# Kernel optimization log

Hardware: AMD Instinct MI355X
Metric: run time of the kernel (lower is better)

Reference implementation:

```python
import jax, jax.numpy as jnp
import numpy as np
from jax import lax

BN_EPS = 1e-5
PAD = ((2, 3), (1, 2))  # 'same' padding for kernel (6,4): H pad 5 -> (2,3), W pad 3 -> (1,2)
DN = ('NCHW', 'OIHW', 'NCHW')


def _conv_block(x, w, b, g, bt, m, v, pool):
    # pool(bn(relu(conv(pad(x))))) as in the torch module (eval-mode BN)
    x = lax.conv_general_dilated(x, w, (1, 1), PAD, dimension_numbers=DN)
    x = jax.nn.relu(x + b[None, :, None, None])
    scale = g / jnp.sqrt(v + BN_EPS)
    x = (x - m[None, :, None, None]) * scale[None, :, None, None] + bt[None, :, None, None]
    win = (1, 1) + pool
    return lax.reduce_window(x, -jnp.inf, lax.max, win, win, 'VALID')


def _fc_bn(x, w, b, g, bt, m, v):
    x = jax.nn.relu(x @ w.T + b)
    return (x - m) * (g / jnp.sqrt(v + BN_EPS)) + bt


def _apply_cnn(x, p):
    x = x[:, None, :, :]  # [N,1,72,64]
    x = _conv_block(x, p['conv1_w'], p['conv1_b'], p['bnc1_g'], p['bnc1_b'], p['bnc1_m'], p['bnc1_v'], (2, 2))
    x = _conv_block(x, p['conv2_w'], p['conv2_b'], p['bnc2_g'], p['bnc2_b'], p['bnc2_m'], p['bnc2_v'], (2, 2))
    x = _conv_block(x, p['conv3_w'], p['conv3_b'], p['bnc3_g'], p['bnc3_b'], p['bnc3_m'], p['bnc3_v'], (3, 4))
    x = x.reshape(x.shape[0], 6 * 4 * 64)  # NCHW contiguous flatten matches torch .view
    x = _fc_bn(x, p['fc1_w'], p['fc1_b'], p['bnf1_g'], p['bnf1_b'], p['bnf1_m'], p['bnf1_v'])
    x = _fc_bn(x, p['fc2_w'], p['fc2_b'], p['bnf2_g'], p['bnf2_b'], p['bnf2_m'], p['bnf2_v'])
    x = _fc_bn(x, p['fc3_w'], p['fc3_b'], p['bnf3_g'], p['bnf3_b'], p['bnf3_m'], p['bnf3_v'])
    # F.normalize(x, p=2, dim=1) with eps=1e-12
    nrm = jnp.linalg.norm(x, axis=1, keepdims=True)
    return x / jnp.maximum(nrm, 1e-12)


def _ssm(embeds):
    # pairwise L2 distances via Gram trick (replaces the O(n^2) python loop)
    sq = jnp.sum(embeds * embeds, axis=1)  # [n]
    d2 = sq[:, None] + sq[None, :] - 2.0 * (embeds @ embeds.T)
    dist = jnp.sqrt(jnp.maximum(d2, 1e-12))
    dist = jnp.where(d2 > 0, dist, 0.0)  # exact zeros on diagonal, nan-safe grad
    return dist / jnp.max(dist)


def setup_inputs() -> dict:
    key = jax.random.key(0)
    ks = iter(jax.random.split(key, 64))
    d = {'x': jax.random.normal(next(ks), (512, 72, 64), jnp.float32)}

    def nrm(shape, s=0.05):
        return jax.random.normal(next(ks), shape, jnp.float32) * s

    def add_bn(name, c):
        d[name + '_g'] = 1.0 + nrm((c,))
        d[name + '_b'] = nrm((c,))
        d[name + '_m'] = nrm((c,), 0.1)
        d[name + '_v'] = 0.5 + jax.random.uniform(next(ks), (c,), jnp.float32)

    d['conv1_w'] = nrm((16, 1, 6, 4), 0.2);  d['conv1_b'] = nrm((16,));  add_bn('bnc1', 16)
    d['conv2_w'] = nrm((32, 16, 6, 4), 0.1); d['conv2_b'] = nrm((32,));  add_bn('bnc2', 32)
    d['conv3_w'] = nrm((64, 32, 6, 4), 0.05); d['conv3_b'] = nrm((64,)); add_bn('bnc3', 64)
    d['fc1_w'] = nrm((512, 1536), 0.03); d['fc1_b'] = nrm((512,)); add_bn('bnf1', 512)
    d['fc2_w'] = nrm((256, 512), 0.05);  d['fc2_b'] = nrm((256,)); add_bn('bnf2', 256)
    d['fc3_w'] = nrm((128, 256), 0.07);  d['fc3_b'] = nrm((128,)); add_bn('bnf3', 128)
    return d


def reference(x,
              conv1_w, conv1_b, bnc1_g, bnc1_b, bnc1_m, bnc1_v,
              conv2_w, conv2_b, bnc2_g, bnc2_b, bnc2_m, bnc2_v,
              conv3_w, conv3_b, bnc3_g, bnc3_b, bnc3_m, bnc3_v,
              fc1_w, fc1_b, bnf1_g, bnf1_b, bnf1_m, bnf1_v,
              fc2_w, fc2_b, bnf2_g, bnf2_b, bnf2_m, bnf2_v,
              fc3_w, fc3_b, bnf3_g, bnf3_b, bnf3_m, bnf3_v):
    p = dict(conv1_w=conv1_w, conv1_b=conv1_b, bnc1_g=bnc1_g, bnc1_b=bnc1_b, bnc1_m=bnc1_m, bnc1_v=bnc1_v,
             conv2_w=conv2_w, conv2_b=conv2_b, bnc2_g=bnc2_g, bnc2_b=bnc2_b, bnc2_m=bnc2_m, bnc2_v=bnc2_v,
             conv3_w=conv3_w, conv3_b=conv3_b, bnc3_g=bnc3_g, bnc3_b=bnc3_b, bnc3_m=bnc3_m, bnc3_v=bnc3_v,
             fc1_w=fc1_w, fc1_b=fc1_b, bnf1_g=bnf1_g, bnf1_b=bnf1_b, bnf1_m=bnf1_m, bnf1_v=bnf1_v,
             fc2_w=fc2_w, fc2_b=fc2_b, bnf2_g=bnf2_g, bnf2_b=bnf2_b, bnf2_m=bnf2_m, bnf2_v=bnf2_v,
             fc3_w=fc3_w, fc3_b=fc3_b, bnf3_g=bnf3_g, bnf3_b=bnf3_b, bnf3_m=bnf3_m, bnf3_v=bnf3_v)
    embeds = _apply_cnn(x, p)  # [n, 128], L2-normalized
    return _ssm(embeds)        # [n, n]
```

## Files before the change

### kernel.cpp

```cpp
#include <hip/hip_runtime.h>
#include <math.h>


#define BN_EPS 1e-5f

typedef __attribute__((ext_vector_type(8))) short short8;
typedef __attribute__((ext_vector_type(4))) float f32x4;

__device__ __forceinline__ unsigned short f2bf(float f) {
    unsigned u = __float_as_uint(f);
    u += 0x7fffu + ((u >> 16) & 1u);
    return (unsigned short)(u >> 16);
}

__global__ __launch_bounds__(256) void repack_k(
    const float* __restrict__ w1, const float* __restrict__ w2,
    const float* __restrict__ w3,
    const float* __restrict__ fw1, const float* __restrict__ fw2,
    const float* __restrict__ fw3,
    unsigned short* __restrict__ wT1b,
    unsigned short* __restrict__ wT2b, unsigned short* __restrict__ wT3b,
    unsigned short* __restrict__ fw1b, unsigned short* __restrict__ fw2b,
    unsigned short* __restrict__ fw3b, unsigned* __restrict__ mxslot)
{
    int t = blockIdx.x * 256 + threadIdx.x;
    if (t == 0) *mxslot = 0u;
    if (t < 512) {
        int k = t & 31, oc = t >> 5;
        wT1b[t] = (k < 24) ? f2bf(w1[oc * 24 + k]) : (unsigned short)0;
    }
    if (t < 12288) {
        int k = t & 31, oc = (t >> 5) & 31, kk = t >> 10;
        int ky = kk >> 1, kxp = kk & 1;
        int hi = k >> 4, ic = k & 15;
        int kx = 2 * kxp + hi;
        wT2b[t] = f2bf(w2[((oc * 16 + ic) * 6 + ky) * 4 + kx]);
    }
    if (t < 49152) {
        int ic = t & 31, oc = (t >> 5) & 63, kk = t >> 11;
        int ky = kk >> 2, kx = kk & 3;
        wT3b[t] = f2bf(w3[((oc * 32 + ic) * 6 + ky) * 4 + kx]);
    }
    if (t < 786432) fw1b[t] = f2bf(fw1[t]);
    if (t < 131072) fw2b[t] = f2bf(fw2[t]);
    if (t < 32768)  fw3b[t] = f2bf(fw3[t]);
}

__global__ __launch_bounds__(512) void conv_all(
    const float* __restrict__ x, const unsigned short* __restrict__ wT1,
    const unsigned short* __restrict__ wT2, const unsigned short* __restrict__ wT3,
    const float* __restrict__ c1b, const float* __restrict__ g1,
    const float* __restrict__ b1, const float* __restrict__ m1,
    const float* __restrict__ v1,
    const float* __restrict__ c2b, const float* __restrict__ g2,
    const float* __restrict__ b2, const float* __restrict__ m2,
    const float* __restrict__ v2,
    const float* __restrict__ c3b, const float* __restrict__ g3,
    const float* __restrict__ b3, const float* __restrict__ m3,
    const float* __restrict__ v3,
    unsigned short* __restrict__ out3)
{
    __shared__ __align__(16) unsigned short s_out1[41 * 36 * 16];
    __shared__ __align__(16) unsigned short s_un[24 * 20 * 32];
    const int tid = threadIdx.x, nl = blockIdx.x;
    const int lane = tid & 63, wave = tid >> 6;
    const int n = lane & 15, q = lane >> 4;
    unsigned short* pa = s_un;
    unsigned short* pb = s_un + 5372;

    {
        unsigned* z32 = (unsigned*)s_un;
        for (int i = tid; i < 5372; i += 512) z32[i] = 0u;
        uint4 z4; z4.x = z4.y = z4.z = z4.w = 0u;
        for (int pc = tid; pc < 324; pc += 512) {
            int row, colc;
            if (pc < 180) { row = pc / 36; colc = pc % 36; if (row >= 2) row += 36; }
            else { int pz = pc - 180; row = 2 + (pz >> 2); colc = (pz & 3) ? 32 + (pz & 3) : 0; }
            uint4* d = (uint4*)(s_out1 + ((size_t)row * 36 + colc) * 16);
            d[0] = z4; d[1] = z4;
        }
    }
    __syncthreads();
    {
        const float4* src = (const float4*)(x + (size_t)nl * 4608);
        for (int i = tid; i < 1152; i += 512) {
            float4 val = src[i];
            int f = i * 4, row = (f >> 6) + 2, c = (f & 63) + 1;
            unsigned short h0 = f2bf(val.x), h1 = f2bf(val.y);
            unsigned short h2 = f2bf(val.z), h3 = f2bf(val.w);
            unsigned short* ap = pa + row * 68 + c;
            ap[0] = h0; ap[1] = h1; ap[2] = h2; ap[3] = h3;
            unsigned* bp = (unsigned*)(pb + row * 68 + c + 1);
            bp[0] = (unsigned)h0 | ((unsigned)h1 << 16);
            bp[1] = (unsigned)h2 | ((unsigned)h3 << 16);
        }
    }
    const float sc1 = g1[n] * rsqrtf(v1[n] + BN_EPS);
    const float bb1 = c1b[n];
    const float mm1 = b1[n] - m1[n] * sc1;
    const short8 bfr1 = *(const short8*)(wT1 + n * 32 + q * 8);
    __syncthreads();

    for (int i = 0; i < 36; ++i) {
        int t = wave * 36 + i;
        int pooled = 4 * t + (n >> 2);
        int ph = pooled >> 5, pw = pooled & 31;
        int py = (n >> 1) & 1, px = n & 1;
        int oh = 2 * ph + py, ow = 2 * pw + px;
        int r0 = (oh + 2 * q) * 68;
        const unsigned* base = px ? (const unsigned*)(pb + r0 + ow + 1)
                                  : (const unsigned*)(pa + r0 + ow);
        uint4 uu;
        uu.x = base[0];  uu.y = base[1];
        uu.z = base[34]; uu.w = base[35];
        short8 afr = *reinterpret_cast<short8*>(&uu);
        f32x4 acc = (f32x4){0.f, 0.f, 0.f, 0.f};
        acc = __builtin_amdgcn_mfma_f32_16x16x32_bf16(afr, bfr1, acc, 0, 0, 0);
        int po = 4 * t + q, oph = po >> 5, opw = po & 31;
        float mx = fmaxf(fmaxf(acc[0], acc[1]), fmaxf(acc[2], acc[3]));
        float val = fmaxf(mx + bb1, 0.f) * sc1 + mm1;
        s_out1[((oph + 2) * 36 + (opw + 1)) * 16 + n] = f2bf(val);
    }
    __syncthreads();
    {
        uint4 z4; z4.x = z4.y = z4.z = z4.w = 0u;
        for (int pc = tid; pc < 192; pc += 512) {
            int row, colc;
            if (pc < 120) { row = pc / 20; colc = pc % 20; if (row >= 2) row += 18; }
            else { int pz = pc - 120; row = 2 + (pz >> 2); colc = (pz & 3) ? 16 + (pz & 3) : 0; }
            uint4* d = (uint4*)(s_un + ((size_t)row * 20 + colc) * 32);
            d[0] = z4; d[1] = z4; d[2] = z4; d[3] = z4;
        }
    }
    float bnb2[2], bns2[2], bnm2[2];
#pragma unroll
    for (int nt = 0; nt < 2; ++nt) {
        int oc = nt * 16 + n;
        float sc = g2[oc] * rsqrtf(v2[oc] + BN_EPS);
        bnb2[nt] = c2b[oc]; bns2[nt] = sc; bnm2[nt] = b2[oc] - m2[oc] * sc;
    }
    __syncthreads();

    for (int pp = wave; pp < 36; pp += 8) {
        int ph = pp >> 1, half = pp & 1;
        f32x4 acc[2][2];
#pragma unroll
        for (int ab = 0; ab < 2; ++ab)
#pragma unroll
            for (int nt = 0; nt < 2; ++nt) acc[ab][nt] = (f32x4){0.f, 0.f, 0.f, 0.f};
#pragma unroll
        for (int ky = 0; ky < 6; ++ky)
#pragma unroll
            for (int kxp = 0; kxp < 2; ++kxp) {
                int kk = ky * 2 + kxp;
                short8 w0 = *(const short8*)(wT2 + ((size_t)(kk * 32 + n) * 32) + q * 8);
                short8 w1 = *(const short8*)(wT2 + ((size_t)(kk * 32 + 16 + n) * 32) + q * 8);
                int col = half * 16 + n + 2 * kxp;
#pragma unroll
                for (int ab = 0; ab < 2; ++ab) {
                    int row = 2 * ph + ab + ky;
                    short8 afr = *(const short8*)(s_out1 + ((size_t)(row * 36 + col) * 16) + q * 8);
                    acc[ab][0] = __builtin_amdgcn_mfma_f32_16x16x32_bf16(afr, w0, acc[ab][0], 0, 0, 0);
                    acc[ab][1] = __builtin_amdgcn_mfma_f32_16x16x32_bf16(afr, w1, acc[ab][1], 0, 0, 0);
                }
            }
        int pw0 = half * 8 + q * 2;
#pragma unroll
        for (int nt = 0; nt < 2; ++nt) {
            int oc = nt * 16 + n;
            float p0 = fmaxf(fmaxf(acc[0][nt][0], acc[0][nt][1]),
                             fmaxf(acc[1][nt][0], acc[1][nt][1]));
            float p1 = fmaxf(fmaxf(acc[0][nt][2], acc[0][nt][3]),
                             fmaxf(acc[1][nt][2], acc[1][nt][3]));
            p0 = fmaxf(p0 + bnb2[nt], 0.f) * bns2[nt] + bnm2[nt];
            p1 = fmaxf(p1 + bnb2[nt], 0.f) * bns2[nt] + bnm2[nt];
            s_un[((size_t)(ph + 2) * 20 + (pw0 + 1)) * 32 + oc] = f2bf(p0);
            s_un[((size_t)(ph + 2) * 20 + (pw0 + 2)) * 32 + oc] = f2bf(p1);
        }
    }
    __syncthreads();

    for (int ch = wave; ch < 12; ch += 8) {
        int pr = ch >> 1, nth = ch & 1;
        f32x4 acc[3][2];
#pragma unroll
        for (int r = 0; r < 3; ++r)
#pragma unroll
            for (int t2 = 0; t2 < 2; ++t2) acc[r][t2] = (f32x4){0.f, 0.f, 0.f, 0.f};
#pragma unroll
        for (int ky = 0; ky < 6; ++ky)
#pragma unroll
            for (int kx = 0; kx < 4; ++kx) {
                int kk = ky * 4 + kx;
                short8 w0 = *(const short8*)(wT3 + ((size_t)(kk * 64 + nth * 32 + n) * 32) + q * 8);
                short8 w1 = *(const short8*)(wT3 + ((size_t)(kk * 64 + nth * 32 + 16 + n) * 32) + q * 8);
#pragma unroll
                for (int r = 0; r < 3; ++r) {
                    int row = 3 * pr + r + ky;
                    int col = n + kx;
                    short8 afr = *(const short8*)(s_un + ((size_t)(row * 20 + col) * 32) + q * 8);
                    acc[r][0] = __builtin_amdgcn_mfma_f32_16x16x32_bf16(afr, w0, acc[r][0], 0, 0, 0);
                    acc[r][1] = __builtin_amdgcn_mfma_f32_16x16x32_bf16(afr, w1, acc[r][1], 0, 0, 0);
                }
            }
        size_t ob = (size_t)nl * 1536;
#pragma unroll
        for (int t2 = 0; t2 < 2; ++t2) {
            int oc = nth * 32 + t2 * 16 + n;
            float sc = g3[oc] * rsqrtf(v3[oc] + BN_EPS);
            float mx = -3.4e38f;
#pragma unroll
            for (int r = 0; r < 3; ++r)
#pragma unroll
                for (int e = 0; e < 4; ++e) mx = fmaxf(mx, acc[r][t2][e]);
            float val = fmaxf(mx + c3b[oc], 0.f) * sc + (b3[oc] - m3[oc] * sc);
            out3[ob + (size_t)oc * 24 + pr * 4 + q] = f2bf(val);
        }
    }
}

__global__ __launch_bounds__(256) void fc_m(
    const unsigned short* __restrict__ A, const unsigned short* __restrict__ W,
    const float* __restrict__ bias, const float* __restrict__ g,
    const float* __restrict__ bt, const float* __restrict__ m,
    const float* __restrict__ v, unsigned short* __restrict__ out_b,
    float* __restrict__ out_f, int K, int N, int mode)
{
    const int tid = threadIdx.x;
    const int lane = tid & 63, wave = tid >> 6;
    const int n = lane & 15, q = lane >> 4;
    const int wr = wave >> 1, wc = wave & 1;
    const int r0 = blockIdx.y * 32 + wr * 16;
    const int c0 = blockIdx.x * 32 + wc * 16;
    const int col = c0 + n;

    float sc = g[col] * rsqrtf(v[col] + BN_EPS);
    float bb = bias[col];
    float mm = bt[col] - m[col] * sc;

    const unsigned short* Ap = A + (size_t)(r0 + n) * K + q * 8;
    const unsigned short* Bp = W + (size_t)col * K + q * 8;

    f32x4 acc = (f32x4){0.f, 0.f, 0.f, 0.f};
    for (int kk = 0; kk < K; kk += 64) {
        short8 a0 = *(const short8*)(Ap + kk);
        short8 b0 = *(const short8*)(Bp + kk);
        short8 a1 = *(const short8*)(Ap + kk + 32);
        short8 b1 = *(const short8*)(Bp + kk + 32);
        acc = __builtin_amdgcn_mfma_f32_16x16x32_bf16(a0, b0, acc, 0, 0, 0);
        acc = __builtin_amdgcn_mfma_f32_16x16x32_bf16(a1, b1, acc, 0, 0, 0);
    }
#pragma unroll
    for (int e = 0; e < 4; ++e) {
        int row = r0 + q * 4 + e;
        float val = fmaxf(acc[e] + bb, 0.f) * sc + mm;
        if (mode == 0) out_b[(size_t)row * N + col] = f2bf(val);
        else           out_f[(size_t)row * N + col] = val;
    }
}

__global__ __launch_bounds__(128) void norm_k(const float* __restrict__ f3,
                                              float* __restrict__ E,
                                              float* __restrict__ sq)
{
    __shared__ float red[2];
    const int row = blockIdx.x, tid = threadIdx.x;
    float vv = f3[row * 128 + tid];
    float s = vv * vv;
#pragma unroll
    for (int off = 32; off >= 1; off >>= 1) s += __shfl_down(s, off, 64);
    if ((tid & 63) == 0) red[tid >> 6] = s;
    __syncthreads();
    float total = red[0] + red[1];
    float nn = fmaxf(sqrtf(total), 1e-12f);
    E[row * 128 + tid] = vv / nn;
    if (tid == 0) sq[row] = total / (nn * nn);
}

__global__ __launch_bounds__(256) void dist_k(const float* __restrict__ E,
                                              const float* __restrict__ sq,
                                              float* __restrict__ D,
                                              unsigned* __restrict__ mxslot)
{
    __shared__ __align__(16) float Ei[16 * 132];
    __shared__ __align__(16) float Ej[16 * 132];
    __shared__ float red[256];
    const int tid = threadIdx.x;
    const int bi = blockIdx.y * 16, bj = blockIdx.x * 16;
    {
        int lr = tid >> 4, lc = (tid & 15) * 8;
        float4 a0 = *(const float4*)(E + (bi + lr) * 128 + lc);
        float4 a1 = *(const float4*)(E + (bi + lr) * 128 + lc + 4);
        *(float4*)(Ei + lr * 132 + lc) = a0;
        *(float4*)(Ei + lr * 132 + lc + 4) = a1;
        float4 b0 = *(const float4*)(E + (bj + lr) * 128 + lc);
        float4 b1 = *(const float4*)(E + (bj + lr) * 128 + lc + 4);
        *(float4*)(Ej + lr * 132 + lc) = b0;
        *(float4*)(Ej + lr * 132 + lc + 4) = b1;
    }
    __syncthreads();
    const int tx = tid & 15, ty = tid >> 4;
    float dot = 0.f;
#pragma unroll 4
    for (int k = 0; k < 128; k += 4) {
        float4 a = *(const float4*)(Ei + ty * 132 + k);
        float4 b = *(const float4*)(Ej + tx * 132 + k);
        dot = fmaf(a.x, b.x, dot); dot = fmaf(a.y, b.y, dot);
        dot = fmaf(a.z, b.z, dot); dot = fmaf(a.w, b.w, dot);
    }
    int i = bi + ty, j = bj + tx;
    float d2 = sq[i] + sq[j] - 2.f * dot;
    float dist = sqrtf(fmaxf(d2, 1e-12f));
    dist = (d2 > 0.f) ? dist : 0.f;
    if (i == j) dist = 0.f;
    D[i * 512 + j] = dist;
    red[tid] = dist;
    __syncthreads();
    for (int s2 = 128; s2 > 0; s2 >>= 1) {
        if (tid < s2) red[tid] = fmaxf(red[tid], red[tid + s2]);
        __syncthreads();
    }
    if (tid == 0) atomicMax(mxslot, __float_as_uint(red[0]));
}

__global__ __launch_bounds__(256) void scale_k(float* __restrict__ D,
                                               const unsigned* __restrict__ mxslot)
{
    int idx = blockIdx.x * 256 + threadIdx.x;
    float M = __uint_as_float(*mxslot);
    D[idx] = D[idx] / M;
}

extern "C" void kernel_launch(void* const* d_in, const int* in_sizes, int n_in,
                              void* d_out, int out_size, void* d_ws, size_t ws_size,
                              hipStream_t stream)
{
    (void)in_sizes; (void)n_in; (void)out_size; (void)ws_size;
    const float* x    = (const float*)d_in[0];
    const float* c1w  = (const float*)d_in[1];
    const float* c1b  = (const float*)d_in[2];
    const float* g1   = (const float*)d_in[3];
    const float* b1   = (const float*)d_in[4];
    const float* m1   = (const float*)d_in[5];
    const float* v1   = (const float*)d_in[6];
    const float* c2w  = (const float*)d_in[7];
    const float* c2b  = (const float*)d_in[8];
    const float* g2   = (const float*)d_in[9];
    const float* b2   = (const float*)d_in[10];
    const float* m2   = (const float*)d_in[11];
    const float* v2   = (const float*)d_in[12];
    const float* c3w  = (const float*)d_in[13];
    const float* c3b  = (const float*)d_in[14];
    const float* g3   = (const float*)d_in[15];
    const float* b3   = (const float*)d_in[16];
    const float* m3   = (const float*)d_in[17];
    const float* v3   = (const float*)d_in[18];
    const float* fw1  = (const float*)d_in[19];
    const float* fb1  = (const float*)d_in[20];
    const float* gf1  = (const float*)d_in[21];
    const float* bf1  = (const float*)d_in[22];
    const float* mf1  = (const float*)d_in[23];
    const float* vf1  = (const float*)d_in[24];
    const float* fw2  = (const float*)d_in[25];
    const float* fb2  = (const float*)d_in[26];
    const float* gf2  = (const float*)d_in[27];
    const float* bf2  = (const float*)d_in[28];
    const float* mf2  = (const float*)d_in[29];
    const float* vf2  = (const float*)d_in[30];
    const float* fw3  = (const float*)d_in[31];
    const float* fb3  = (const float*)d_in[32];
    const float* gf3  = (const float*)d_in[33];
    const float* bf3  = (const float*)d_in[34];
    const float* mf3  = (const float*)d_in[35];
    const float* vf3  = (const float*)d_in[36];

    float* ws = (float*)d_ws;
    float* E    = ws + 0;
    float* sq   = ws + 65536;
    float* f3v  = ws + 66048;
    unsigned* mx = (unsigned*)(ws + 131584);
    unsigned short* wT1b = (unsigned short*)(ws + 131600);
    unsigned short* wT2b = (unsigned short*)(ws + 131856);
    unsigned short* wT3b = (unsigned short*)(ws + 138000);
    unsigned short* fw1b = (unsigned short*)(ws + 162576);
    unsigned short* fw2b = (unsigned short*)(ws + 555792);
    unsigned short* fw3b = (unsigned short*)(ws + 621328);
    unsigned short* out3b= (unsigned short*)(ws + 637712);
    unsigned short* a1b  = (unsigned short*)(ws + 1030928);
    unsigned short* a2b  = (unsigned short*)(ws + 1162000);

    float* out = (float*)d_out;

    repack_k<<<3072, 256, 0, stream>>>(c1w, c2w, c3w, fw1, fw2, fw3,
                                       wT1b, wT2b, wT3b, fw1b, fw2b, fw3b, mx);
    conv_all<<<512, 512, 0, stream>>>(x, wT1b, wT2b, wT3b,
                                      c1b, g1, b1, m1, v1,
                                      c2b, g2, b2, m2, v2,
                                      c3b, g3, b3, m3, v3, out3b);
    fc_m<<<dim3(16, 16), 256, 0, stream>>>(out3b, fw1b, fb1, gf1, bf1, mf1, vf1,
                                           a1b, nullptr, 1536, 512, 0);
    fc_m<<<dim3(8, 16), 256, 0, stream>>>(a1b, fw2b, fb2, gf2, bf2, mf2, vf2,
                                          a2b, nullptr, 512, 256, 0);
    fc_m<<<dim3(4, 16), 256, 0, stream>>>(a2b, fw3b, fb3, gf3, bf3, mf3, vf3,
                                          nullptr, f3v, 256, 128, 1);
    norm_k<<<512, 128, 0, stream>>>(f3v, E, sq);
    dist_k<<<dim3(32, 32), 256, 0, stream>>>(E, sq, out, mx);
    scale_k<<<1024, 256, 0, stream>>>(out, mx);
}
```

Measured before the change: 219.6 us.

## Convert FC weights in-kernel, fuse fc3 with normalize, swizzle conv3 LDS, resize conv block

Stops pre-converting the large FC weight matrices to bf16 in the repack kernel. The FC kernels now read fp32 weights and pack them to bf16 in registers, which removes a big write and re-read pass over the weights. The final FC layer is fused with L2 normalisation into one kernel, which drops the separate norm launch and its intermediate buffer. The conv kernel moves from 512 to 384 threads, with work redistributed per wave and an XOR-swizzled LDS layout for conv2's output / conv3's input to avoid bank conflicts. The cost is extra global fp32 weight traffic and conversion work repeated in every FC block, since each weight tile is read by many row blocks.

New measurement: 229.2 us. 1.04x slower.

```diff
diff --git a/kernel.cpp b/kernel.cpp
--- a/kernel.cpp
+++ b/kernel.cpp
@@ -1,4 +1,5 @@
 #include <hip/hip_runtime.h>
+#include <hip/hip_bf16.h>
 #include <math.h>
 
 
@@ -13,15 +14,21 @@
     return (unsigned short)(u >> 16);
 }
 
+__device__ __forceinline__ unsigned pkbf(float a, float b) {
+    __hip_bfloat162 h = __float22bfloat162_rn(make_float2(a, b));
+    return *reinterpret_cast<unsigned*>(&h);
+}
+
+__device__ __forceinline__ int sw2(int c, int h) {
+    return c * 32 + ((h ^ (c & 3) ^ ((c >> 2) & 3)) << 3);
+}
+
 __global__ __launch_bounds__(256) void repack_k(
     const float* __restrict__ w1, const float* __restrict__ w2,
     const float* __restrict__ w3,
-    const float* __restrict__ fw1, const float* __restrict__ fw2,
-    const float* __restrict__ fw3,
     unsigned short* __restrict__ wT1b,
     unsigned short* __restrict__ wT2b, unsigned short* __restrict__ wT3b,
-    unsigned short* __restrict__ fw1b, unsigned short* __restrict__ fw2b,
-    unsigned short* __restrict__ fw3b, unsigned* __restrict__ mxslot)
+    unsigned* __restrict__ mxslot)
 {
     int t = blockIdx.x * 256 + threadIdx.x;
     if (t == 0) *mxslot = 0u;
@@ -41,12 +48,9 @@
         int ky = kk >> 2, kx = kk & 3;
         wT3b[t] = f2bf(w3[((oc * 32 + ic) * 6 + ky) * 4 + kx]);
     }
-    if (t < 786432) fw1b[t] = f2bf(fw1[t]);
-    if (t < 131072) fw2b[t] = f2bf(fw2[t]);
-    if (t < 32768)  fw3b[t] = f2bf(fw3[t]);
-}
-
-__global__ __launch_bounds__(512) void conv_all(
+}
+
+__global__ __launch_bounds__(384) void conv_all(
     const float* __restrict__ x, const unsigned short* __restrict__ wT1,
     const unsigned short* __restrict__ wT2, const unsigned short* __restrict__ wT3,
     const float* __restrict__ c1b, const float* __restrict__ g1,
@@ -70,9 +74,9 @@
 
     {
         unsigned* z32 = (unsigned*)s_un;
-        for (int i = tid; i < 5372; i += 512) z32[i] = 0u;
+        for (int i = tid; i < 5372; i += 384) z32[i] = 0u;
         uint4 z4; z4.x = z4.y = z4.z = z4.w = 0u;
-        for (int pc = tid; pc < 324; pc += 512) {
+        for (int pc = tid; pc < 324; pc += 384) {
             int row, colc;
             if (pc < 180) { row = pc / 36; colc = pc % 36; if (row >= 2) row += 36; }
             else { int pz = pc - 180; row = 2 + (pz >> 2); colc = (pz & 3) ? 32 + (pz & 3) : 0; }
@@ -83,7 +87,7 @@
     __syncthreads();
     {
         const float4* src = (const float4*)(x + (size_t)nl * 4608);
-        for (int i = tid; i < 1152; i += 512) {
+        for (int i = tid; i < 1152; i += 384) {
             float4 val = src[i];
             int f = i * 4, row = (f >> 6) + 2, c = (f & 63) + 1;
             unsigned short h0 = f2bf(val.x), h1 = f2bf(val.y);
@@ -101,8 +105,8 @@
     const short8 bfr1 = *(const short8*)(wT1 + n * 32 + q * 8);
     __syncthreads();
 
-    for (int i = 0; i < 36; ++i) {
-        int t = wave * 36 + i;
+    for (int i = 0; i < 48; ++i) {
+        int t = wave * 48 + i;
         int pooled = 4 * t + (n >> 2);
         int ph = pooled >> 5, pw = pooled & 31;
         int py = (n >> 1) & 1, px = n & 1;
@@ -124,7 +128,7 @@
     __syncthreads();
     {
         uint4 z4; z4.x = z4.y = z4.z = z4.w = 0u;
-        for (int pc = tid; pc < 192; pc += 512) {
+        for (int pc = tid; pc < 192; pc += 384) {
             int row, colc;
             if (pc < 120) { row = pc / 20; colc = pc % 20; if (row >= 2) row += 18; }
             else { int pz = pc - 120; row = 2 + (pz >> 2); colc = (pz & 3) ? 16 + (pz & 3) : 0; }
@@ -141,7 +145,7 @@
     }
     __syncthreads();
 
-    for (int pp = wave; pp < 36; pp += 8) {
+    for (int pp = wave; pp < 36; pp += 6) {
         int ph = pp >> 1, half = pp & 1;
         f32x4 acc[2][2];
 #pragma unroll
@@ -174,57 +178,50 @@
                              fmaxf(acc[1][nt][2], acc[1][nt][3]));
             p0 = fmaxf(p0 + bnb2[nt], 0.f) * bns2[nt] + bnm2[nt];
             p1 = fmaxf(p1 + bnb2[nt], 0.f) * bns2[nt] + bnm2[nt];
-            s_un[((size_t)(ph + 2) * 20 + (pw0 + 1)) * 32 + oc] = f2bf(p0);
-            s_un[((size_t)(ph + 2) * 20 + (pw0 + 2)) * 32 + oc] = f2bf(p1);
+            int c1 = (ph + 2) * 20 + (pw0 + 1);
+            s_un[sw2(c1, oc >> 3) + (oc & 7)] = f2bf(p0);
+            s_un[sw2(c1 + 1, oc >> 3) + (oc & 7)] = f2bf(p1);
         }
     }
     __syncthreads();
 
-    for (int ch = wave; ch < 12; ch += 8) {
-        int pr = ch >> 1, nth = ch & 1;
-        f32x4 acc[3][2];
-#pragma unroll
-        for (int r = 0; r < 3; ++r)
-#pragma unroll
-            for (int t2 = 0; t2 < 2; ++t2) acc[r][t2] = (f32x4){0.f, 0.f, 0.f, 0.f};
+    for (int u = wave; u < 24; u += 6) {
+        int pr = u >> 2, nt4 = u & 3;
+        f32x4 acc[3];
+#pragma unroll
+        for (int r = 0; r < 3; ++r) acc[r] = (f32x4){0.f, 0.f, 0.f, 0.f};
 #pragma unroll
         for (int ky = 0; ky < 6; ++ky)
 #pragma unroll
             for (int kx = 0; kx < 4; ++kx) {
                 int kk = ky * 4 + kx;
-                short8 w0 = *(const short8*)(wT3 + ((size_t)(kk * 64 + nth * 32 + n) * 32) + q * 8);
-                short8 w1 = *(const short8*)(wT3 + ((size_t)(kk * 64 + nth * 32 + 16 + n) * 32) + q * 8);
+                short8 w0 = *(const short8*)(wT3 + ((size_t)(kk * 64 + nt4 * 16 + n) * 32) + q * 8);
 #pragma unroll
                 for (int r = 0; r < 3; ++r) {
                     int row = 3 * pr + r + ky;
-                    int col = n + kx;
-                    short8 afr = *(const short8*)(s_un + ((size_t)(row * 20 + col) * 32) + q * 8);
-                    acc[r][0] = __builtin_amdgcn_mfma_f32_16x16x32_bf16(afr, w0, acc[r][0], 0, 0, 0);
-                    acc[r][1] = __builtin_amdgcn_mfma_f32_16x16x32_bf16(afr, w1, acc[r][1], 0, 0, 0);
+                    int c = row * 20 + n + kx;
+                    short8 afr = *(const short8*)(s_un + sw2(c, q));
+                    acc[r] = __builtin_amdgcn_mfma_f32_16x16x32_bf16(afr, w0, acc[r], 0, 0, 0);
                 }
             }
-        size_t ob = (size_t)nl * 1536;
-#pragma unroll
-        for (int t2 = 0; t2 < 2; ++t2) {
-            int oc = nth * 32 + t2 * 16 + n;
-            float sc = g3[oc] * rsqrtf(v3[oc] + BN_EPS);
-            float mx = -3.4e38f;
-#pragma unroll
-            for (int r = 0; r < 3; ++r)
-#pragma unroll
-                for (int e = 0; e < 4; ++e) mx = fmaxf(mx, acc[r][t2][e]);
-            float val = fmaxf(mx + c3b[oc], 0.f) * sc + (b3[oc] - m3[oc] * sc);
-            out3[ob + (size_t)oc * 24 + pr * 4 + q] = f2bf(val);
-        }
+        int oc = nt4 * 16 + n;
+        float sc = g3[oc] * rsqrtf(v3[oc] + BN_EPS);
+        float mx = -3.4e38f;
+#pragma unroll
+        for (int r = 0; r < 3; ++r)
+#pragma unroll
+            for (int e = 0; e < 4; ++e) mx = fmaxf(mx, acc[r][e]);
+        float val = fmaxf(mx + c3b[oc], 0.f) * sc + (b3[oc] - m3[oc] * sc);
+        out3[(size_t)nl * 1536 + (size_t)oc * 24 + pr * 4 + q] = f2bf(val);
     }
 }
 
 __global__ __launch_bounds__(256) void fc_m(
-    const unsigned short* __restrict__ A, const unsigned short* __restrict__ W,
+    const unsigned short* __restrict__ A, const float* __restrict__ Wf,
     const float* __restrict__ bias, const float* __restrict__ g,
     const float* __restrict__ bt, const float* __restrict__ m,
     const float* __restrict__ v, unsigned short* __restrict__ out_b,
-    float* __restrict__ out_f, int K, int N, int mode)
+    int K, int N)
 {
     const int tid = threadIdx.x;
     const int lane = tid & 63, wave = tid >> 6;
@@ -239,14 +236,23 @@
     float mm = bt[col] - m[col] * sc;
 
     const unsigned short* Ap = A + (size_t)(r0 + n) * K + q * 8;
-    const unsigned short* Bp = W + (size_t)col * K + q * 8;
+    const float* Bp = Wf + (size_t)col * K + q * 8;
 
     f32x4 acc = (f32x4){0.f, 0.f, 0.f, 0.f};
     for (int kk = 0; kk < K; kk += 64) {
         short8 a0 = *(const short8*)(Ap + kk);
-        short8 b0 = *(const short8*)(Bp + kk);
         short8 a1 = *(const short8*)(Ap + kk + 32);
-        short8 b1 = *(const short8*)(Bp + kk + 32);
+        float4 f0 = *(const float4*)(Bp + kk);
+        float4 f1 = *(const float4*)(Bp + kk + 4);
+        float4 f2 = *(const float4*)(Bp + kk + 32);
+        float4 f3 = *(const float4*)(Bp + kk + 36);
+        uint4 u0, u1;
+        u0.x = pkbf(f0.x, f0.y); u0.y = pkbf(f0.z, f0.w);
+        u0.z = pkbf(f1.x, f1.y); u0.w = pkbf(f1.z, f1.w);
+        u1.x = pkbf(f2.x, f2.y); u1.y = pkbf(f2.z, f2.w);
+        u1.z = pkbf(f3.x, f3.y); u1.w = pkbf(f3.z, f3.w);
+        short8 b0 = *reinterpret_cast<short8*>(&u0);
+        short8 b1 = *reinterpret_cast<short8*>(&u1);
         acc = __builtin_amdgcn_mfma_f32_16x16x32_bf16(a0, b0, acc, 0, 0, 0);
         acc = __builtin_amdgcn_mfma_f32_16x16x32_bf16(a1, b1, acc, 0, 0, 0);
     }
@@ -254,27 +260,73 @@
     for (int e = 0; e < 4; ++e) {
         int row = r0 + q * 4 + e;
         float val = fmaxf(acc[e] + bb, 0.f) * sc + mm;
-        if (mode == 0) out_b[(size_t)row * N + col] = f2bf(val);
-        else           out_f[(size_t)row * N + col] = val;
-    }
-}
-
-__global__ __launch_bounds__(128) void norm_k(const float* __restrict__ f3,
-                                              float* __restrict__ E,
-                                              float* __restrict__ sq)
-{
-    __shared__ float red[2];
-    const int row = blockIdx.x, tid = threadIdx.x;
-    float vv = f3[row * 128 + tid];
-    float s = vv * vv;
-#pragma unroll
-    for (int off = 32; off >= 1; off >>= 1) s += __shfl_down(s, off, 64);
-    if ((tid & 63) == 0) red[tid >> 6] = s;
-    __syncthreads();
-    float total = red[0] + red[1];
-    float nn = fmaxf(sqrtf(total), 1e-12f);
-    E[row * 128 + tid] = vv / nn;
-    if (tid == 0) sq[row] = total / (nn * nn);
+        out_b[(size_t)row * N + col] = f2bf(val);
+    }
+}
+
+__global__ __launch_bounds__(512) void fc3norm_k(
+    const unsigned short* __restrict__ A, const float* __restrict__ Wf,
+    const float* __restrict__ bias, const float* __restrict__ g,
+    const float* __restrict__ bt, const float* __restrict__ m,
+    const float* __restrict__ v,
+    float* __restrict__ E, float* __restrict__ sq)
+{
+    __shared__ __align__(16) float z3[16 * 128];
+    const int tid = threadIdx.x;
+    const int lane = tid & 63, wave = tid >> 6;
+    const int n = lane & 15, q = lane >> 4;
+    const int r0 = blockIdx.x * 16;
+    const int col = wave * 16 + n;
+
+    float sc = g[col] * rsqrtf(v[col] + BN_EPS);
+    float bb = bias[col];
+    float mm = bt[col] - m[col] * sc;
+
+    const unsigned short* Ap = A + (size_t)(r0 + n) * 256 + q * 8;
+    const float* Bp = Wf + (size_t)col * 256 + q * 8;
+
+    f32x4 acc = (f32x4){0.f, 0.f, 0.f, 0.f};
+    for (int kk = 0; kk < 256; kk += 64) {
+        short8 a0 = *(const short8*)(Ap + kk);
+        short8 a1 = *(const short8*)(Ap + kk + 32);
+        float4 f0 = *(const float4*)(Bp + kk);
+        float4 f1 = *(const float4*)(Bp + kk + 4);
+        float4 f2 = *(const float4*)(Bp + kk + 32);
+        float4 f3 = *(const float4*)(Bp + kk + 36);
+        uint4 u0, u1;
+        u0.x = pkbf(f0.x, f0.y); u0.y = pkbf(f0.z, f0.w);
+        u0.z = pkbf(f1.x, f1.y); u0.w = pkbf(f1.z, f1.w);
+        u1.x = pkbf(f2.x, f2.y); u1.y = pkbf(f2.z, f2.w);
+        u1.z = pkbf(f3.x, f3.y); u1.w = pkbf(f3.z, f3.w);
+        short8 b0 = *reinterpret_cast<short8*>(&u0);
+        short8 b1 = *reinterpret_cast<short8*>(&u1);
+        acc = __builtin_amdgcn_mfma_f32_16x16x32_bf16(a0, b0, acc, 0, 0, 0);
+        acc = __builtin_amdgcn_mfma_f32_16x16x32_bf16(a1, b1, acc, 0, 0, 0);
+    }
+#pragma unroll
+    for (int e = 0; e < 4; ++e) {
+        float val = fmaxf(acc[e] + bb, 0.f) * sc + mm;
+        z3[(q * 4 + e) * 128 + col] = val;
+    }
+    __syncthreads();
+    if (tid < 256) {
+        int row_l = tid >> 4, j = tid & 15;
+        float4 v0 = *(const float4*)(z3 + row_l * 128 + j * 8);
+        float4 v1 = *(const float4*)(z3 + row_l * 128 + j * 8 + 4);
+        float s = v0.x * v0.x + v0.y * v0.y + v0.z * v0.z + v0.w * v0.w
+                + v1.x * v1.x + v1.y * v1.y + v1.z * v1.z + v1.w * v1.w;
+#pragma unroll
+        for (int off = 1; off < 16; off <<= 1) s += __shfl_xor(s, off, 16);
+        float nn = fmaxf(sqrtf(s), 1e-12f);
+        float inv = 1.f / nn;
+        int row = r0 + row_l;
+        float4 e0, e1;
+        e0.x = v0.x * inv; e0.y = v0.y * inv; e0.z = v0.z * inv; e0.w = v0.w * inv;
+        e1.x = v1.x * inv; e1.y = v1.y * inv; e1.z = v1.z * inv; e1.w = v1.w * inv;
+        *(float4*)(E + (size_t)row * 128 + j * 8) = e0;
+        *(float4*)(E + (size_t)row * 128 + j * 8 + 4) = e1;
+        if (j == 0) sq[row] = s * inv * inv;
+    }
 }
 
 __global__ __launch_bounds__(256) void dist_k(const float* __restrict__ E,
@@ -377,33 +429,26 @@
     float* ws = (float*)d_ws;
     float* E    = ws + 0;
     float* sq   = ws + 65536;
-    float* f3v  = ws + 66048;
-    unsigned* mx = (unsigned*)(ws + 131584);
-    unsigned short* wT1b = (unsigned short*)(ws + 131600);
-    unsigned short* wT2b = (unsigned short*)(ws + 131856);
-    unsigned short* wT3b = (unsigned short*)(ws + 138000);
-    unsigned short* fw1b = (unsigned short*)(ws + 162576);
-    unsigned short* fw2b = (unsigned short*)(ws + 555792);
-    unsigned short* fw3b = (unsigned short*)(ws + 621328);
-    unsigned short* out3b= (unsigned short*)(ws + 637712);
-    unsigned short* a1b  = (unsigned short*)(ws + 1030928);
-    unsigned short* a2b  = (unsigned short*)(ws + 1162000);
+    unsigned* mx = (unsigned*)(ws + 66048);
+    unsigned short* wT1b = (unsigned short*)(ws + 66064);
+    unsigned short* wT2b = (unsigned short*)(ws + 66320);
+    unsigned short* wT3b = (unsigned short*)(ws + 72464);
+    unsigned short* out3b= (unsigned short*)(ws + 97040);
+    unsigned short* a1b  = (unsigned short*)(ws + 490256);
+    unsigned short* a2b  = (unsigned short*)(ws + 621328);
 
     float* out = (float*)d_out;
 
-    repack_k<<<3072, 256, 0, stream>>>(c1w, c2w, c3w, fw1, fw2, fw3,
-                                       wT1b, wT2b, wT3b, fw1b, fw2b, fw3b, mx);
-    conv_all<<<512, 512, 0, stream>>>(x, wT1b, wT2b, wT3b,
+    repack_k<<<192, 256, 0, stream>>>(c1w, c2w, c3w, wT1b, wT2b, wT3b, mx);
+    conv_all<<<512, 384, 0, stream>>>(x, wT1b, wT2b, wT3b,
                                       c1b, g1, b1, m1, v1,
                                       c2b, g2, b2, m2, v2,
                                       c3b, g3, b3, m3, v3, out3b);
-    fc_m<<<dim3(16, 16), 256, 0, stream>>>(out3b, fw1b, fb1, gf1, bf1, mf1, vf1,
-                                           a1b, nullptr, 1536, 512, 0);
-    fc_m<<<dim3(8, 16), 256, 0, stream>>>(a1b, fw2b, fb2, gf2, bf2, mf2, vf2,
-                                          a2b, nullptr, 512, 256, 0);
-    fc_m<<<dim3(4, 16), 256, 0, stream>>>(a2b, fw3b, fb3, gf3, bf3, mf3, vf3,
-                                          nullptr, f3v, 256, 128, 1);
-    norm_k<<<512, 128, 0, stream>>>(f3v, E, sq);
+    fc_m<<<dim3(16, 16), 256, 0, stream>>>(out3b, fw1, fb1, gf1, bf1, mf1, vf1,
+                                           a1b, 1536, 512);
+    fc_m<<<dim3(8, 16), 256, 0, stream>>>(a1b, fw2, fb2, gf2, bf2, mf2, vf2,
+                                          a2b, 512, 256);
+    fc3norm_k<<<32, 512, 0, stream>>>(a2b, fw3, fb3, gf3, bf3, mf3, vf3, E, sq);
     dist_k<<<dim3(32, 32), 256, 0, stream>>>(E, sq, out, mx);
     scale_k<<<1024, 256, 0, stream>>>(out, mx);
 }
```
